# Optimization experiments

Hardware: AMD Instinct MI355X
Metric: run time of the kernel (lower is better)

## Reference

```python
import jax, jax.numpy as jnp
import numpy as np

LIMIT = 0.01  # codebook init range, per module's `limit` arg


def setup_inputs() -> dict:
    key = jax.random.key(0)
    k1, k2 = jax.random.split(key)
    B, T, D, K = 64, 1024, 256, 4096
    x = jax.random.normal(k1, (B, T, D), dtype=jnp.float32)
    # codebook: (embedding_dim, num_embeddings), uniform in [-limit, limit]
    vectors = jax.random.uniform(k2, (D, K), dtype=jnp.float32, minval=-LIMIT, maxval=LIMIT)
    return {"x": x, "vectors": vectors}


def reference(x, vectors):
    D = x.shape[-1]
    flat_x = x.reshape(-1, D)  # (N, D)
    # squared euclidean distances to each codebook vector: (N, K)
    distances = ((flat_x ** 2).sum(axis=1, keepdims=True)
                 - 2.0 * flat_x @ vectors
                 + (vectors ** 2).sum(axis=0, keepdims=True))
    encoding_indices = jnp.argmin(distances, axis=1)  # (N,)
    # gather nearest codebook vectors: vectors.T is (K, D)
    quantized_x = jnp.take(vectors.T, encoding_indices, axis=0).reshape(x.shape)
    dictionary_loss = jnp.mean((jax.lax.stop_gradient(x) - quantized_x) ** 2)
    commitment_loss = jnp.mean((x - jax.lax.stop_gradient(quantized_x)) ** 2)
    # straight-through estimator
    quantized_st = x + jax.lax.stop_gradient(quantized_x - x)
    return (quantized_st, dictionary_loss, commitment_loss,
            encoding_indices.reshape(x.shape[0], -1))
```

## Files before the change

### kernel.cpp

```cpp
#include <hip/hip_runtime.h>
#include <cfloat>

#define NROWS 65536
#define DIM   256
#define KCB   4096

typedef __attribute__((ext_vector_type(8))) short bf16x8;
typedef __attribute__((ext_vector_type(4))) float f32x4;
typedef unsigned short ushort;
typedef unsigned int uint;


__device__ __forceinline__ bool better(float v1, int i1, float v2, int i2) {
    return (v1 < v2) || (v1 == v2 && i1 < i2);
}

__device__ __forceinline__ float opaque(float x) {
    asm volatile("" : "+v"(x));
    return x;
}

__device__ __forceinline__ ushort f2bf(float f) {
    uint u = __float_as_uint(f);
    return (ushort)((u + 0x7FFFu + ((u >> 16) & 1u)) >> 16);
}

__device__ __forceinline__ void insert4b(float v[4], int idx[4], float s, int k) {
    if (better(s, k, v[3], idx[3])) {
        if (better(s, k, v[2], idx[2])) {
            v[3] = v[2]; idx[3] = idx[2];
            if (better(s, k, v[1], idx[1])) {
                v[2] = v[1]; idx[2] = idx[1];
                if (better(s, k, v[0], idx[0])) {
                    v[1] = v[0]; idx[1] = idx[0]; v[0] = s; idx[0] = k;
                } else { v[1] = s; idx[1] = k; }
            } else { v[2] = s; idx[2] = k; }
        } else { v[3] = s; idx[3] = k; }
    }
}

__global__ void vq_cref_kernel(const float* __restrict__ v,
                               float* __restrict__ cref) {
    int k = blockIdx.x * blockDim.x + threadIdx.x;
    float t = v[k];
    float c = opaque(t * t);
    for (int d = 1; d < DIM; ++d) {
        t = v[d * KCB + k];
        c = c + opaque(t * t);
    }
    cref[k] = c;
}

__global__ void vq_transpose_kernel(const float* __restrict__ v,
                                    float* __restrict__ vt) {
    __shared__ float tile[32][33];
    int d0 = blockIdx.x * 32;
    int k0 = blockIdx.y * 32;
    int tx = threadIdx.x;
    int ty = threadIdx.y;
    #pragma unroll
    for (int i = 0; i < 32; i += 8)
        tile[ty + i][tx] = v[(d0 + ty + i) * KCB + k0 + tx];
    __syncthreads();
    #pragma unroll
    for (int i = 0; i < 32; i += 8)
        vt[(k0 + ty + i) * DIM + d0 + tx] = tile[tx][ty + i];
}

__global__ __launch_bounds__(256) void vq_pack_kernel(const float* __restrict__ vt,
                                                      ushort* __restrict__ vthp) {
    int t = blockIdx.x * 256 + threadIdx.x;
    int lane = t & 63;
    int dt   = (t >> 6) & 7;
    int g    = t >> 9;
    int row  = g * 16 + (lane & 15);
    int dbase = (dt * 4 + (lane >> 4)) * 8;
    const float* src = vt + (size_t)row * DIM + dbase;
    float4 f0 = *(const float4*)src;
    float4 f1 = *(const float4*)(src + 4);
    int4 p;
    p.x = (int)f2bf(f0.x) | ((int)f2bf(f0.y) << 16);
    p.y = (int)f2bf(f0.z) | ((int)f2bf(f0.w) << 16);
    p.z = (int)f2bf(f1.x) | ((int)f2bf(f1.y) << 16);
    p.w = (int)f2bf(f1.z) | ((int)f2bf(f1.w) << 16);
    *(int4*)(vthp + (size_t)t * 8) = p;
}

__global__ __launch_bounds__(256, 4) void vq_mfma_argmin_kernel(
        const float* __restrict__ x, const ushort* __restrict__ vthp,
        const float* __restrict__ cref, int4* __restrict__ cand) {
    __shared__ __align__(16) ushort Bk[32 * 64 * 8];

    const int tid  = threadIdx.x;
    const int w    = tid >> 6;
    const int lane = tid & 63;
    const int l15  = lane & 15;
    const int quad = lane >> 4;
    const int row0 = blockIdx.x * 64;

    {
        const int r_ = tid >> 2;
        const int q_ = tid & 3;
        const float* xs = &x[(size_t)(row0 + r_) * DIM + q_ * 64];
        #pragma unroll
        for (int i = 0; i < 8; ++i) {
            float4 f0 = *(const float4*)(xs + i * 8);
            float4 f1 = *(const float4*)(xs + i * 8 + 4);
            int4 p;
            p.x = (int)f2bf(f0.x) | ((int)f2bf(f0.y) << 16);
            p.y = (int)f2bf(f0.z) | ((int)f2bf(f0.w) << 16);
            p.z = (int)f2bf(f1.x) | ((int)f2bf(f1.y) << 16);
            p.w = (int)f2bf(f1.z) | ((int)f2bf(f1.w) << 16);
            int u = q_ * 8 + i;
            *(int4*)&Bk[(u * 64 + r_) * 8] = p;
        }
    }
    __syncthreads();

    float m0[4], m1[4];
    #pragma unroll
    for (int nj = 0; nj < 4; ++nj) { m0[nj] = FLT_MAX; m1[nj] = FLT_MAX; }

    for (int kt = 0; kt < 16; ++kt) {
        f32x4 acc[4][4];
        #pragma unroll
        for (int mi = 0; mi < 4; ++mi)
            #pragma unroll
            for (int nj = 0; nj < 4; ++nj)
                acc[mi][nj] = (f32x4)0.f;

        const ushort* akt = vthp
            + ((size_t)(kt * 16 + w * 4) * 8 * 64 + lane) * 8;

        #pragma unroll 2
        for (int dt = 0; dt < 8; ++dt) {
            bf16x8 af[4], bfr[4];
            #pragma unroll
            for (int mi = 0; mi < 4; ++mi)
                af[mi] = *(const bf16x8*)(akt + mi * 4096 + dt * 512);
            #pragma unroll
            for (int nj = 0; nj < 4; ++nj)
                bfr[nj] = *(const bf16x8*)&Bk[((dt * 4 + quad) * 64 + nj * 16 + l15) * 8];
            #pragma unroll
            for (int mi = 0; mi < 4; ++mi)
                #pragma unroll
                for (int nj = 0; nj < 4; ++nj)
                    acc[mi][nj] = __builtin_amdgcn_mfma_f32_16x16x32_bf16(
                        af[mi], bfr[nj], acc[mi][nj], 0, 0, 0);
        }

        const uint ktb = (uint)(kt << 4);
        float4 cv[4];
        #pragma unroll
        for (int mi = 0; mi < 4; ++mi)
            cv[mi] = *(const float4*)&cref[kt * 256 + w * 64 + mi * 16 + quad * 4];

        #pragma unroll
        for (int nj = 0; nj < 4; ++nj) {
            #pragma unroll
            for (int mi = 0; mi < 4; ++mi) {
                #pragma unroll
                for (int r = 0; r < 4; ++r) {
                    float s = fmaf(-2.f, acc[mi][nj][r], (&cv[mi].x)[r]);
                    uint  pk = (__float_as_uint(s) & 0xFFFFFF00u)
                             | (ktb + (uint)(mi * 4 + r));
                    float f = __uint_as_float(pk);
                    m1[nj] = __builtin_amdgcn_fmed3f(f, m0[nj], m1[nj]);
                    m0[nj] = fminf(m0[nj], f);
                }
            }
        }
    }

    float mv[4][4];
    int   mi_[4][4];
    #pragma unroll
    for (int nj = 0; nj < 4; ++nj) {
        uint b0 = __float_as_uint(m0[nj]);
        uint b1 = __float_as_uint(m1[nj]);
        int id0 = (int)(b0 & 255u);
        int id1 = (int)(b1 & 255u);
        mv[nj][0] = m0[nj];
        mi_[nj][0] = ((id0 >> 4) << 8) + w * 64 + (((id0 >> 2) & 3) << 4)
                   + (quad << 2) + (id0 & 3);
        mv[nj][1] = m1[nj];
        mi_[nj][1] = ((id1 >> 4) << 8) + w * 64 + (((id1 >> 2) & 3) << 4)
                   + (quad << 2) + (id1 & 3);
        mv[nj][2] = FLT_MAX; mi_[nj][2] = 0;
        mv[nj][3] = FLT_MAX; mi_[nj][3] = 0;
    }
    #pragma unroll
    for (int off = 16; off <= 32; off <<= 1) {
        #pragma unroll
        for (int nj = 0; nj < 4; ++nj) {
            float ov[4]; int oi[4];
            #pragma unroll
            for (int s = 0; s < 4; ++s) {
                ov[s] = __shfl_xor(mv[nj][s], off);
                oi[s] = __shfl_xor(mi_[nj][s], off);
            }
            #pragma unroll
            for (int s = 0; s < 4; ++s)
                insert4b(mv[nj], mi_[nj], ov[s], oi[s]);
        }
    }

    __syncthreads();
    float2* mbuf = (float2*)Bk;
    if (quad == 0) {
        #pragma unroll
        for (int nj = 0; nj < 4; ++nj) {
            int row_local = nj * 16 + l15;
            #pragma unroll
            for (int s = 0; s < 4; ++s)
                mbuf[row_local * 16 + w * 4 + s] =
                    make_float2(mv[nj][s], __int_as_float(mi_[nj][s]));
        }
    }
    __syncthreads();
    if (tid < 64) {
        float bv[4] = {FLT_MAX, FLT_MAX, FLT_MAX, FLT_MAX};
        int   bi[4] = {0, 0, 0, 0};
        #pragma unroll
        for (int j = 0; j < 16; ++j) {
            float2 p = mbuf[tid * 16 + j];
            insert4b(bv, bi, p.x, __float_as_int(p.y));
        }
        cand[row0 + tid] = make_int4(bi[0], bi[1], bi[2], bi[3]);
    }
}

__global__ __launch_bounds__(256) void vq_emuquant_kernel(
        const float* __restrict__ x, const float* __restrict__ vt,
        const float* __restrict__ cref, const int4* __restrict__ cand,
        float* __restrict__ out_q, float* __restrict__ out_idx,
        float* __restrict__ partial) {
    __shared__ float rsum[64];

    int gid = blockIdx.x * blockDim.x + threadIdx.x;
    int row = gid >> 2;
    int cl  = gid & 3;
    int c   = ((const int*)cand)[gid];

    const float4* xr = (const float4*)(x + (size_t)row * DIM);
    const float4* vr = (const float4*)(vt + (size_t)c * DIM);

    float b = 0.f;
    float A_half[2];
    #pragma unroll
    for (int h = 0; h < 2; ++h) {
        float r[8];
        for (int i = 0; i < 16; ++i) {
            float4 xa = xr[h * 32 + i * 2];
            float4 xb = xr[h * 32 + i * 2 + 1];
            float4 va = vr[h * 32 + i * 2];
            float4 vb = vr[h * 32 + i * 2 + 1];
            float xs[8] = {xa.x, xa.y, xa.z, xa.w, xb.x, xb.y, xb.z, xb.w};
            float vs[8] = {va.x, va.y, va.z, va.w, vb.x, vb.y, vb.z, vb.w};
            if (i == 0) {
                #pragma unroll
                for (int j = 0; j < 8; ++j) {
                    r[j] = opaque(xs[j] * xs[j]);
                    b = fmaf(2.f * xs[j], vs[j], b);
                }
            } else {
                #pragma unroll
                for (int j = 0; j < 8; ++j) {
                    r[j] = r[j] + opaque(xs[j] * xs[j]);
                    b = fmaf(2.f * xs[j], vs[j], b);
                }
            }
        }
        A_half[h] = ((r[0] + r[1]) + (r[2] + r[3])) + ((r[4] + r[5]) + (r[6] + r[7]));
    }
    float A = A_half[0] + A_half[1];

    float bd = (A - b) + cref[c];
    int   bk = c;
    #pragma unroll
    for (int off = 1; off <= 2; off <<= 1) {
        float ov = __shfl_xor(bd, off);
        int   oi = __shfl_xor(bk, off);
        if (better(ov, oi, bd, bk)) { bd = ov; bk = oi; }
    }
    if (cl == 0) out_idx[row] = (float)bk;

    {
        const float* xs = x     + (size_t)row * DIM + cl * 64;
        const float* vs = vt    + (size_t)bk  * DIM + cl * 64;
        float*       qs = out_q + (size_t)row * DIM + cl * 64;
        float lsum = 0.f;
        #pragma unroll
        for (int i = 0; i < 16; ++i) {
            float4 xv = *(const float4*)(xs + i * 4);
            float4 qv = *(const float4*)(vs + i * 4);
            *(float4*)(qs + i * 4) = qv;
            float dx = xv.x - qv.x, dy = xv.y - qv.y;
            float dz = xv.z - qv.z, dw = xv.w - qv.w;
            lsum += dx * dx + dy * dy + dz * dz + dw * dw;
        }
        lsum += __shfl_xor(lsum, 1);
        lsum += __shfl_xor(lsum, 2);
        if (cl == 0) rsum[threadIdx.x >> 2] = lsum;
    }
    __syncthreads();
    if (threadIdx.x < 64) {
        float s = rsum[threadIdx.x];
        #pragma unroll
        for (int off = 32; off > 0; off >>= 1)
            s += __shfl_xor(s, off);
        if (threadIdx.x == 0) partial[blockIdx.x] = s;
    }
}

__global__ void vq_finalize_kernel(const float* __restrict__ partial,
                                   float* __restrict__ out_loss) {
    __shared__ double sd[256];
    double s = 0.0;
    for (int i = threadIdx.x; i < 1024; i += 256)
        s += (double)partial[i];
    sd[threadIdx.x] = s;
    __syncthreads();
    for (int off = 128; off > 0; off >>= 1) {
        if (threadIdx.x < off) sd[threadIdx.x] += sd[threadIdx.x + off];
        __syncthreads();
    }
    if (threadIdx.x == 0) {
        double m = sd[0] / (double)((long long)NROWS * DIM);
        out_loss[0] = (float)m;
        out_loss[1] = (float)m;
    }
}

extern "C" void kernel_launch(void* const* d_in, const int* in_sizes, int n_in,
                              void* d_out, int out_size, void* d_ws, size_t ws_size,
                              hipStream_t stream) {
    const float* x = (const float*)d_in[0];
    const float* v = (const float*)d_in[1];

    float* out      = (float*)d_out;
    float* out_q    = out;
    float* out_loss = out + (size_t)NROWS * DIM;
    float* out_idx  = out + (size_t)NROWS * DIM + 2;

    char*   ws      = (char*)d_ws;
    float*  cref    = (float*)ws;
    int4*   cand    = (int4*)(ws + 32768);
    float*  partial = (float*)(ws + 1081344);
    float*  vt      = (float*)(ws + 1343488);
    ushort* vthp    = (ushort*)(ws + 5537792);

    vq_cref_kernel<<<KCB / 256, 256, 0, stream>>>(v, cref);
    vq_transpose_kernel<<<dim3(DIM / 32, KCB / 32), dim3(32, 8), 0, stream>>>(v, vt);
    vq_pack_kernel<<<512, 256, 0, stream>>>(vt, vthp);
    vq_mfma_argmin_kernel<<<NROWS / 64, 256, 0, stream>>>(x, vthp, cref, cand);
    vq_emuquant_kernel<<<NROWS * 4 / 256, 256, 0, stream>>>(x, vt, cref, cand,
                                                            out_q, out_idx, partial);
    vq_finalize_kernel<<<1, 256, 0, stream>>>(partial, out_loss);
}
```

Measured before the change: 416.6 us.

## Stage candidate codebook rows through LDS for coalesced loads in emuquant kernel

The rescoring kernel now loads each wave's candidate codebook rows cooperatively, with 16 lanes reading one row contiguously, into a swizzled LDS staging buffer. Each thread then reads its own row from LDS instead of doing strided per-thread global loads. The output-write and loss pass is reorganised so a whole wave handles one row at a time with coalesced float4 accesses, and the cref loop gets an unroll pragma. The cost is 64KB of LDS per block, which may limit occupancy, plus extra waits on the LDS counter.

```diff
diff --git a/kernel.cpp b/kernel.cpp
--- a/kernel.cpp
+++ b/kernel.cpp
@@ -44,6 +44,7 @@
     int k = blockIdx.x * blockDim.x + threadIdx.x;
     float t = v[k];
     float c = opaque(t * t);
+    #pragma unroll 8
     for (int d = 1; d < DIM; ++d) {
         t = v[d * KCB + k];
         c = c + opaque(t * t);
@@ -235,39 +236,70 @@
         const float* __restrict__ cref, const int4* __restrict__ cand,
         float* __restrict__ out_q, float* __restrict__ out_idx,
         float* __restrict__ partial) {
-    __shared__ float rsum[64];
-
-    int gid = blockIdx.x * blockDim.x + threadIdx.x;
-    int row = gid >> 2;
-    int cl  = gid & 3;
-    int c   = ((const int*)cand)[gid];
+    __shared__ __align__(16) float stage[4][4096];
+
+    const int tid  = threadIdx.x;
+    const int w    = tid >> 6;
+    const int lane = tid & 63;
+    const int gid  = blockIdx.x * 256 + tid;
+    const int row  = gid >> 2;
+    const int cl   = gid & 3;
+
+    float* stW = stage[w];
+    float* myBase = stW + lane * 64;
+    const int swz = lane & 31;
+
+    const int c_mine = ((const int*)cand)[gid];
+    const int* cbase = (const int*)cand + blockIdx.x * 256 + w * 64;
 
     const float4* xr = (const float4*)(x + (size_t)row * DIM);
-    const float4* vr = (const float4*)(vt + (size_t)c * DIM);
 
     float b = 0.f;
     float A_half[2];
     #pragma unroll
     for (int h = 0; h < 2; ++h) {
         float r[8];
-        for (int i = 0; i < 16; ++i) {
-            float4 xa = xr[h * 32 + i * 2];
-            float4 xb = xr[h * 32 + i * 2 + 1];
-            float4 va = vr[h * 32 + i * 2];
-            float4 vb = vr[h * 32 + i * 2 + 1];
-            float xs[8] = {xa.x, xa.y, xa.z, xa.w, xb.x, xb.y, xb.z, xb.w};
-            float vs[8] = {va.x, va.y, va.z, va.w, vb.x, vb.y, vb.z, vb.w};
-            if (i == 0) {
+        #pragma unroll
+        for (int iq = 0; iq < 2; ++iq) {
+            const int qq = h * 2 + iq;
+            asm volatile("s_waitcnt lgkmcnt(0)" ::: "memory");
+            #pragma unroll
+            for (int it = 0; it < 16; ++it) {
+                int j  = it * 4 + (lane >> 4);
+                int cj = cbase[j];
+                float4 vv = *(const float4*)(vt + (size_t)cj * DIM
+                                             + qq * 64 + (lane & 15) * 4);
+                int f0 = (lane & 15) * 4;
+                int jx = j & 31;
+                float* dst = stW + j * 64;
+                dst[(f0 + 0) ^ jx] = vv.x;
+                dst[(f0 + 1) ^ jx] = vv.y;
+                dst[(f0 + 2) ^ jx] = vv.z;
+                dst[(f0 + 3) ^ jx] = vv.w;
+            }
+            asm volatile("s_waitcnt lgkmcnt(0)" ::: "memory");
+            #pragma unroll
+            for (int il = 0; il < 8; ++il) {
+                const int i = iq * 8 + il;
+                float4 xa = xr[h * 32 + i * 2];
+                float4 xb = xr[h * 32 + i * 2 + 1];
+                float xs[8] = {xa.x, xa.y, xa.z, xa.w, xb.x, xb.y, xb.z, xb.w};
+                float vs[8];
                 #pragma unroll
-                for (int j = 0; j < 8; ++j) {
-                    r[j] = opaque(xs[j] * xs[j]);
-                    b = fmaf(2.f * xs[j], vs[j], b);
-                }
-            } else {
-                #pragma unroll
-                for (int j = 0; j < 8; ++j) {
-                    r[j] = r[j] + opaque(xs[j] * xs[j]);
-                    b = fmaf(2.f * xs[j], vs[j], b);
+                for (int jj = 0; jj < 8; ++jj)
+                    vs[jj] = myBase[(il * 8 + jj) ^ swz];
+                if (i == 0) {
+                    #pragma unroll
+                    for (int jj = 0; jj < 8; ++jj) {
+                        r[jj] = opaque(xs[jj] * xs[jj]);
+                        b = fmaf(2.f * xs[jj], vs[jj], b);
+                    }
+                } else {
+                    #pragma unroll
+                    for (int jj = 0; jj < 8; ++jj) {
+                        r[jj] = r[jj] + opaque(xs[jj] * xs[jj]);
+                        b = fmaf(2.f * xs[jj], vs[jj], b);
+                    }
                 }
             }
         }
@@ -275,8 +307,8 @@
     }
     float A = A_half[0] + A_half[1];
 
-    float bd = (A - b) + cref[c];
-    int   bk = c;
+    float bd = (A - b) + cref[c_mine];
+    int   bk = c_mine;
     #pragma unroll
     for (int off = 1; off <= 2; off <<= 1) {
         float ov = __shfl_xor(bd, off);
@@ -285,32 +317,29 @@
     }
     if (cl == 0) out_idx[row] = (float)bk;
 
-    {
-        const float* xs = x     + (size_t)row * DIM + cl * 64;
-        const float* vs = vt    + (size_t)bk  * DIM + cl * 64;
-        float*       qs = out_q + (size_t)row * DIM + cl * 64;
-        float lsum = 0.f;
-        #pragma unroll
-        for (int i = 0; i < 16; ++i) {
-            float4 xv = *(const float4*)(xs + i * 4);
-            float4 qv = *(const float4*)(vs + i * 4);
-            *(float4*)(qs + i * 4) = qv;
-            float dx = xv.x - qv.x, dy = xv.y - qv.y;
-            float dz = xv.z - qv.z, dw = xv.w - qv.w;
-            lsum += dx * dx + dy * dy + dz * dz + dw * dw;
-        }
-        lsum += __shfl_xor(lsum, 1);
-        lsum += __shfl_xor(lsum, 2);
-        if (cl == 0) rsum[threadIdx.x >> 2] = lsum;
-    }
-    __syncthreads();
-    if (threadIdx.x < 64) {
-        float s = rsum[threadIdx.x];
-        #pragma unroll
-        for (int off = 32; off > 0; off >>= 1)
-            s += __shfl_xor(s, off);
-        if (threadIdx.x == 0) partial[blockIdx.x] = s;
-    }
+    float lsum = 0.f;
+    const int wrow0 = blockIdx.x * 64 + w * 16;
+    #pragma unroll 4
+    for (int rr = 0; rr < 16; ++rr) {
+        int kwin = __shfl(bk, rr * 4);
+        const float* xs = x     + (size_t)(wrow0 + rr) * DIM + lane * 4;
+        const float* vs = vt    + (size_t)kwin * DIM + lane * 4;
+        float*       qs = out_q + (size_t)(wrow0 + rr) * DIM + lane * 4;
+        float4 xv = *(const float4*)xs;
+        float4 qv = *(const float4*)vs;
+        *(float4*)qs = qv;
+        float dx = xv.x - qv.x, dy = xv.y - qv.y;
+        float dz = xv.z - qv.z, dw2 = xv.w - qv.w;
+        lsum += dx * dx + dy * dy + dz * dz + dw2 * dw2;
+    }
+    #pragma unroll
+    for (int off = 32; off > 0; off >>= 1)
+        lsum += __shfl_xor(lsum, off);
+    if (lane == 0) stW[0] = lsum;
+    __syncthreads();
+    if (tid == 0)
+        partial[blockIdx.x] = (stage[0][0] + stage[1][0])
+                            + (stage[2][0] + stage[3][0]);
 }
 
 __global__ void vq_finalize_kernel(const float* __restrict__ partial,
```

Result: slower. 473.6 us (+13.7%).
